# Kernel tuning notes

Measured on AMD Instinct MI355X. Metric: run time of the kernel, lower is better.

## Reference

```python
import jax, jax.numpy as jnp
import numpy as np

NEG_SLOPE = 0.2
F_OUT = 64


def setup_inputs() -> dict:
    key = jax.random.key(0)
    k1, k2, k3 = jax.random.split(key, 3)
    N, F_IN = 8192, 256
    h = jax.random.normal(k1, (N, F_IN), dtype=jnp.float32)
    adj = jnp.ones((N, N), dtype=jnp.bool_)  # unused by the original forward
    # xavier-uniform-ish init scale
    W = jax.random.uniform(k2, (F_IN, F_OUT), dtype=jnp.float32,
                           minval=-1.0, maxval=1.0) * np.sqrt(6.0 / (F_IN + F_OUT))
    a = jax.random.uniform(k3, (2 * F_OUT, 1), dtype=jnp.float32,
                           minval=-1.0, maxval=1.0) * np.sqrt(6.0 / (2 * F_OUT + 1))
    return {"h": h, "adj": adj, "W": W, "a": a}


def reference(h, adj, W, a):
    # Wh: [N, F_OUT]
    Wh = h @ W
    # The torch code materializes an [N*N, F] repeat to compute what is just
    # a broadcast add of two projected score vectors:
    # e[i, j] = leakyrelu(Wh[i] @ a1 + Wh[j] @ a2)
    s1 = Wh @ a[:F_OUT]   # [N, 1]
    s2 = Wh @ a[F_OUT:]   # [N, 1]
    e = s1 + s2.T         # [N, N]
    e = jnp.where(e >= 0, e, NEG_SLOPE * e)  # LeakyReLU(0.2)
    attention = jax.nn.softmax(e, axis=1)    # note: adj is NOT used (matches source)
    return attention @ Wh                    # [N, F_OUT]
```

## Files before the change

### kernel.cpp

```cpp
#include <hip/hip_runtime.h>
#include <math.h>

#define GN 8192
#define GF 64
#define GFIN 256
#define NEG 0.2f
#define NCH 1024
#define CHSZ 8

#define OFF_WH   0
#define OFF_S1   (GN*GF)
#define OFF_S2   (OFF_S1 + GN)
#define OFF_ZS   (OFF_S2 + GN)
#define OFF_IDX  (OFF_ZS + GN)
#define OFF_CHA  (OFF_IDX + GN)
#define OFF_CHB  (OFF_CHA + NCH*GF)
#define OFF_SCA  (OFF_CHB + NCH*GF)
#define OFF_SCB  (OFF_SCA + NCH)
#define OFF_OFA  (OFF_SCB + NCH)
#define OFF_OFB  (OFF_OFA + (NCH+1)*GF)
#define OFF_OSA  (OFF_OFB + (NCH+1)*GF)
#define OFF_OSB  (OFF_OSA + (NCH+1))

__global__ __launch_bounds__(256) void k_wh(const float* __restrict__ h,
        const float* __restrict__ W, const float* __restrict__ a,
        float* __restrict__ Wh, float* __restrict__ s1, float* __restrict__ s2) {
    __shared__ float Wl[GFIN*GF];
    int t = threadIdx.x;
    int lane = t & 63;
    const float4* W4 = (const float4*)W;
    float4* Wl4 = (float4*)Wl;
    #pragma unroll
    for (int m = 0; m < 16; ++m) Wl4[t + m*256] = W4[t + m*256];
    __syncthreads();
    int wid = __builtin_amdgcn_readfirstlane(t >> 6);
    int row0 = blockIdx.x * 32 + wid * 8;
    const float* hrow = h + (size_t)row0 * GFIN;
    float acc[8] = {0.f,0.f,0.f,0.f,0.f,0.f,0.f,0.f};
    #pragma unroll 8
    for (int k = 0; k < GFIN; ++k) {
        float wv = Wl[k*GF + lane];
        #pragma unroll
        for (int q = 0; q < 8; ++q) acc[q] += hrow[q*GFIN + k] * wv;
    }
    float a1 = a[lane], a2 = a[GF + lane];
    #pragma unroll
    for (int q = 0; q < 8; ++q) {
        int row = row0 + q;
        Wh[(size_t)row*GF + lane] = acc[q];
        float v1 = acc[q]*a1, v2 = acc[q]*a2;
        #pragma unroll
        for (int o = 32; o > 0; o >>= 1) { v1 += __shfl_xor(v1, o); v2 += __shfl_xor(v2, o); }
        if (lane == 0) { s1[row] = v1; s2[row] = v2; }
    }
}

__global__ __launch_bounds__(256) void k_rank(const float* __restrict__ s2v,
        float* __restrict__ zs, int* __restrict__ idx) {
    __shared__ float z[GN];
    int t = threadIdx.x;
    const float4* s4 = (const float4*)s2v;
    float4* z4 = (float4*)z;
    for (int m = t; m < GN/4; m += 256) z4[m] = s4[m];
    __syncthreads();
    int jl = t >> 3, s = t & 7;
    int j = blockIdx.x * 32 + jl;
    float zj = z[j];
    int cnt = 0;
    #pragma unroll 4
    for (int i = 0; i < GN/32; ++i) {
        int m4 = i*8 + s;
        float4 v = z4[m4];
        int mb = m4*4;
        cnt += (v.x < zj) || (v.x == zj && mb+0 < j);
        cnt += (v.y < zj) || (v.y == zj && mb+1 < j);
        cnt += (v.z < zj) || (v.z == zj && mb+2 < j);
        cnt += (v.w < zj) || (v.w == zj && mb+3 < j);
    }
    cnt += __shfl_xor(cnt, 1);
    cnt += __shfl_xor(cnt, 2);
    cnt += __shfl_xor(cnt, 4);
    if (s == 0) { zs[cnt] = zj; idx[cnt] = j; }
}

__global__ __launch_bounds__(256) void k_chunk(const float* __restrict__ Wh,
        const float* __restrict__ zs, const int* __restrict__ idx,
        float* __restrict__ chA, float* __restrict__ chB,
        float* __restrict__ scA, float* __restrict__ scB) {
    int t = threadIdx.x;
    int wid = t >> 6, lane = t & 63;
    int ch = blockIdx.x*4 + wid;
    float Z = zs[GN-1];
    float aAcc = 0.f, bAcc = 0.f, sa = 0.f, sb = 0.f;
    #pragma unroll
    for (int q = 0; q < CHSZ; ++q) {
        int r = ch*CHSZ + q;
        float zr = zs[r];
        int ir = idx[r];
        float d = zr - Z;
        float tA = __expf(d);
        float tB = __expf(NEG * d);
        float w = Wh[(size_t)ir*GF + lane];
        aAcc += tA*w; bAcc += tB*w; sa += tA; sb += tB;
    }
    chA[ch*GF + lane] = aAcc;
    chB[ch*GF + lane] = bAcc;
    if (lane == 0) { scA[ch] = sa; scB[ch] = sb; }
}

__global__ __launch_bounds__(256) void k_scan(const float* __restrict__ chA,
        const float* __restrict__ chB, const float* __restrict__ scA,
        const float* __restrict__ scB,
        float* __restrict__ offA, float* __restrict__ offB,
        float* __restrict__ osA, float* __restrict__ osB) {
    __shared__ float wsum[4];
    __shared__ float wsum2[4];
    int c = blockIdx.x;
    int t = threadIdx.x;
    int lane = t & 63, wid = t >> 6;
    float v[4];
    #pragma unroll
    for (int q = 0; q < 4; ++q) {
        int ch = t*4 + q;
        v[q] = (c < 64) ? chB[ch*GF + c] : scB[ch];
    }
    float s = v[0]+v[1]+v[2]+v[3];
    float ws = s;
    #pragma unroll
    for (int o = 1; o < 64; o <<= 1) { float y = __shfl_up(ws, o); if (lane >= o) ws += y; }
    if (lane == 63) wsum[wid] = ws;
    __syncthreads();
    float blkoff = 0.f, tot = 0.f;
    #pragma unroll
    for (int w2 = 0; w2 < 4; ++w2) { float x = wsum[w2]; tot += x; if (w2 < wid) blkoff += x; }
    float base = blkoff + ws - s;
    #pragma unroll
    for (int q = 0; q < 4; ++q) {
        int ch = t*4 + q;
        if (c < 64) offB[ch*GF + c] = base; else osB[ch] = base;
        base += v[q];
    }
    if (t == 0) { if (c < 64) offB[NCH*GF + c] = tot; else osB[NCH] = tot; }
    __syncthreads();
    #pragma unroll
    for (int q = 0; q < 4; ++q) {
        int ch = NCH-1 - (t*4 + q);
        v[q] = (c < 64) ? chA[ch*GF + c] : scA[ch];
    }
    s = v[0]+v[1]+v[2]+v[3];
    ws = s;
    #pragma unroll
    for (int o = 1; o < 64; o <<= 1) { float y = __shfl_up(ws, o); if (lane >= o) ws += y; }
    if (lane == 63) wsum2[wid] = ws;
    __syncthreads();
    blkoff = 0.f;
    #pragma unroll
    for (int w2 = 0; w2 < 4; ++w2) { float x = wsum2[w2]; if (w2 < wid) blkoff += x; }
    base = blkoff + ws - s;
    #pragma unroll
    for (int q = 0; q < 4; ++q) {
        int ch = NCH-1 - (t*4 + q);
        if (c < 64) offA[ch*GF + c] = base; else osA[ch] = base;
        base += v[q];
    }
    if (t == 0) { if (c < 64) offA[NCH*GF + c] = 0.f; else osA[NCH] = 0.f; }
}

__global__ __launch_bounds__(256) void k_out(const float* __restrict__ s1,
        const float* __restrict__ zs, const int* __restrict__ idx,
        const float* __restrict__ Wh,
        const float* __restrict__ offA, const float* __restrict__ offB,
        const float* __restrict__ osA, const float* __restrict__ osB,
        float* __restrict__ out) {
    int t = threadIdx.x;
    int wid = t >> 6, lane = t & 63;
    int i = blockIdx.x*4 + wid;
    float s1i = s1[i];
    float Z = zs[GN-1];
    float g = s1i + Z;
    float m = (g >= 0.f) ? g : NEG*g;
    float aA = __expf(g - m);
    float aB = __expf(NEG*g - m);
    float tgt = -s1i;
    int lo = 0, hi = GN;
    #pragma unroll
    for (int it = 0; it < 13; ++it) {
        int mid = (lo + hi) >> 1;
        if (zs[mid] < tgt) lo = mid + 1; else hi = mid;
    }
    int k = lo;
    int c0 = k >> 3;
    float va, vb, sa, pb;
    if (c0 < NCH) {
        va = offA[c0*GF + lane]; vb = offB[c0*GF + lane];
        sa = osA[c0];            pb = osB[c0];
        #pragma unroll
        for (int q = 0; q < CHSZ; ++q) {
            int r = c0*CHSZ + q;
            float zr = zs[r]; int ir = idx[r];
            float w = Wh[(size_t)ir*GF + lane];
            float d = zr - Z;
            if (r >= k) { float tA = __expf(d);      va += tA*w; sa += tA; }
            else        { float tB = __expf(NEG*d);  vb += tB*w; pb += tB; }
        }
    } else {
        va = 0.f; sa = 0.f;
        vb = offB[NCH*GF + lane]; pb = osB[NCH];
    }
    out[(size_t)i*GF + lane] = (aA*va + aB*vb) / (aA*sa + aB*pb);
}

extern "C" void kernel_launch(void* const* d_in, const int* in_sizes, int n_in,
                              void* d_out, int out_size, void* d_ws, size_t ws_size,
                              hipStream_t stream) {
    const float* h = (const float*)d_in[0];
    const float* W = (const float*)d_in[2];
    const float* a = (const float*)d_in[3];
    float* ws = (float*)d_ws;
    float* Wh  = ws + OFF_WH;
    float* s1  = ws + OFF_S1;
    float* s2  = ws + OFF_S2;
    float* zs  = ws + OFF_ZS;
    int*   idx = (int*)(ws + OFF_IDX);
    float* chA = ws + OFF_CHA;
    float* chB = ws + OFF_CHB;
    float* scA = ws + OFF_SCA;
    float* scB = ws + OFF_SCB;
    float* ofA = ws + OFF_OFA;
    float* ofB = ws + OFF_OFB;
    float* osA = ws + OFF_OSA;
    float* osB = ws + OFF_OSB;
    float* out = (float*)d_out;

    hipLaunchKernelGGL(k_wh,    dim3(GN/32),  dim3(256), 0, stream, h, W, a, Wh, s1, s2);
    hipLaunchKernelGGL(k_rank,  dim3(GN/32),  dim3(256), 0, stream, s2, zs, idx);
    hipLaunchKernelGGL(k_chunk, dim3(NCH/4),  dim3(256), 0, stream, Wh, zs, idx, chA, chB, scA, scB);
    hipLaunchKernelGGL(k_scan,  dim3(65),     dim3(256), 0, stream, chA, chB, scA, scB, ofA, ofB, osA, osB);
    hipLaunchKernelGGL(k_out,   dim3(GN/4),   dim3(256), 0, stream, s1, zs, idx, Wh, ofA, ofB, osA, osB, out);
}
```

Before: 69.81 us.

## Fuse GAT pipeline into one cooperative kernel with grid syncs

Replaces the five separate launches (projection, rank sort, chunk sums, scan, output) with one cooperative kernel of 256 blocks × 512 threads, separated by grid.sync barriers. The sorted score array is kept in LDS and reused for the chunk phase and the output binary search, which now runs with 4 rows per wavefront. Chunk size is halved (2048 chunks of 4) to shorten the per-row tail loop. This removes inter-kernel launch gaps and some global reloads, at the cost of grid-wide barrier overhead and a launch configuration limited to one block per CU.

Result: slower. 185.4 us (+165.6%).

```diff
diff --git a/kernel.cpp b/kernel.cpp
--- a/kernel.cpp
+++ b/kernel.cpp
@@ -1,12 +1,17 @@
 #include <hip/hip_runtime.h>
+#include <hip/hip_cooperative_groups.h>
 #include <math.h>
+
+namespace cg = cooperative_groups;
 
 #define GN 8192
 #define GF 64
 #define GFIN 256
 #define NEG 0.2f
-#define NCH 1024
-#define CHSZ 8
+#define NBLK 256
+#define TPB 512
+#define NCH 2048
+#define CHSZ 4
 
 #define OFF_WH   0
 #define OFF_S1   (GN*GF)
@@ -22,192 +27,203 @@
 #define OFF_OSA  (OFF_OFB + (NCH+1)*GF)
 #define OFF_OSB  (OFF_OSA + (NCH+1))
 
-__global__ __launch_bounds__(256) void k_wh(const float* __restrict__ h,
-        const float* __restrict__ W, const float* __restrict__ a,
-        float* __restrict__ Wh, float* __restrict__ s1, float* __restrict__ s2) {
-    __shared__ float Wl[GFIN*GF];
-    int t = threadIdx.x;
-    int lane = t & 63;
-    const float4* W4 = (const float4*)W;
-    float4* Wl4 = (float4*)Wl;
-    #pragma unroll
-    for (int m = 0; m < 16; ++m) Wl4[t + m*256] = W4[t + m*256];
-    __syncthreads();
-    int wid = __builtin_amdgcn_readfirstlane(t >> 6);
-    int row0 = blockIdx.x * 32 + wid * 8;
-    const float* hrow = h + (size_t)row0 * GFIN;
-    float acc[8] = {0.f,0.f,0.f,0.f,0.f,0.f,0.f,0.f};
-    #pragma unroll 8
-    for (int k = 0; k < GFIN; ++k) {
-        float wv = Wl[k*GF + lane];
-        #pragma unroll
-        for (int q = 0; q < 8; ++q) acc[q] += hrow[q*GFIN + k] * wv;
-    }
-    float a1 = a[lane], a2 = a[GF + lane];
-    #pragma unroll
-    for (int q = 0; q < 8; ++q) {
-        int row = row0 + q;
-        Wh[(size_t)row*GF + lane] = acc[q];
-        float v1 = acc[q]*a1, v2 = acc[q]*a2;
-        #pragma unroll
-        for (int o = 32; o > 0; o >>= 1) { v1 += __shfl_xor(v1, o); v2 += __shfl_xor(v2, o); }
-        if (lane == 0) { s1[row] = v1; s2[row] = v2; }
-    }
-}
-
-__global__ __launch_bounds__(256) void k_rank(const float* __restrict__ s2v,
-        float* __restrict__ zs, int* __restrict__ idx) {
-    __shared__ float z[GN];
-    int t = threadIdx.x;
-    const float4* s4 = (const float4*)s2v;
-    float4* z4 = (float4*)z;
-    for (int m = t; m < GN/4; m += 256) z4[m] = s4[m];
-    __syncthreads();
-    int jl = t >> 3, s = t & 7;
-    int j = blockIdx.x * 32 + jl;
-    float zj = z[j];
-    int cnt = 0;
-    #pragma unroll 4
-    for (int i = 0; i < GN/32; ++i) {
-        int m4 = i*8 + s;
-        float4 v = z4[m4];
-        int mb = m4*4;
-        cnt += (v.x < zj) || (v.x == zj && mb+0 < j);
-        cnt += (v.y < zj) || (v.y == zj && mb+1 < j);
-        cnt += (v.z < zj) || (v.z == zj && mb+2 < j);
-        cnt += (v.w < zj) || (v.w == zj && mb+3 < j);
-    }
-    cnt += __shfl_xor(cnt, 1);
-    cnt += __shfl_xor(cnt, 2);
-    cnt += __shfl_xor(cnt, 4);
-    if (s == 0) { zs[cnt] = zj; idx[cnt] = j; }
-}
-
-__global__ __launch_bounds__(256) void k_chunk(const float* __restrict__ Wh,
-        const float* __restrict__ zs, const int* __restrict__ idx,
-        float* __restrict__ chA, float* __restrict__ chB,
-        float* __restrict__ scA, float* __restrict__ scB) {
-    int t = threadIdx.x;
-    int wid = t >> 6, lane = t & 63;
-    int ch = blockIdx.x*4 + wid;
-    float Z = zs[GN-1];
-    float aAcc = 0.f, bAcc = 0.f, sa = 0.f, sb = 0.f;
-    #pragma unroll
-    for (int q = 0; q < CHSZ; ++q) {
-        int r = ch*CHSZ + q;
-        float zr = zs[r];
-        int ir = idx[r];
-        float d = zr - Z;
-        float tA = __expf(d);
-        float tB = __expf(NEG * d);
-        float w = Wh[(size_t)ir*GF + lane];
-        aAcc += tA*w; bAcc += tB*w; sa += tA; sb += tB;
-    }
-    chA[ch*GF + lane] = aAcc;
-    chB[ch*GF + lane] = bAcc;
-    if (lane == 0) { scA[ch] = sa; scB[ch] = sb; }
-}
-
-__global__ __launch_bounds__(256) void k_scan(const float* __restrict__ chA,
-        const float* __restrict__ chB, const float* __restrict__ scA,
-        const float* __restrict__ scB,
-        float* __restrict__ offA, float* __restrict__ offB,
-        float* __restrict__ osA, float* __restrict__ osB) {
-    __shared__ float wsum[4];
-    __shared__ float wsum2[4];
-    int c = blockIdx.x;
-    int t = threadIdx.x;
-    int lane = t & 63, wid = t >> 6;
-    float v[4];
-    #pragma unroll
-    for (int q = 0; q < 4; ++q) {
-        int ch = t*4 + q;
-        v[q] = (c < 64) ? chB[ch*GF + c] : scB[ch];
-    }
-    float s = v[0]+v[1]+v[2]+v[3];
-    float ws = s;
-    #pragma unroll
-    for (int o = 1; o < 64; o <<= 1) { float y = __shfl_up(ws, o); if (lane >= o) ws += y; }
-    if (lane == 63) wsum[wid] = ws;
-    __syncthreads();
-    float blkoff = 0.f, tot = 0.f;
-    #pragma unroll
-    for (int w2 = 0; w2 < 4; ++w2) { float x = wsum[w2]; tot += x; if (w2 < wid) blkoff += x; }
-    float base = blkoff + ws - s;
-    #pragma unroll
-    for (int q = 0; q < 4; ++q) {
-        int ch = t*4 + q;
-        if (c < 64) offB[ch*GF + c] = base; else osB[ch] = base;
-        base += v[q];
-    }
-    if (t == 0) { if (c < 64) offB[NCH*GF + c] = tot; else osB[NCH] = tot; }
-    __syncthreads();
-    #pragma unroll
-    for (int q = 0; q < 4; ++q) {
-        int ch = NCH-1 - (t*4 + q);
-        v[q] = (c < 64) ? chA[ch*GF + c] : scA[ch];
-    }
-    s = v[0]+v[1]+v[2]+v[3];
-    ws = s;
-    #pragma unroll
-    for (int o = 1; o < 64; o <<= 1) { float y = __shfl_up(ws, o); if (lane >= o) ws += y; }
-    if (lane == 63) wsum2[wid] = ws;
-    __syncthreads();
-    blkoff = 0.f;
-    #pragma unroll
-    for (int w2 = 0; w2 < 4; ++w2) { float x = wsum2[w2]; if (w2 < wid) blkoff += x; }
-    base = blkoff + ws - s;
-    #pragma unroll
-    for (int q = 0; q < 4; ++q) {
-        int ch = NCH-1 - (t*4 + q);
-        if (c < 64) offA[ch*GF + c] = base; else osA[ch] = base;
-        base += v[q];
-    }
-    if (t == 0) { if (c < 64) offA[NCH*GF + c] = 0.f; else osA[NCH] = 0.f; }
-}
-
-__global__ __launch_bounds__(256) void k_out(const float* __restrict__ s1,
-        const float* __restrict__ zs, const int* __restrict__ idx,
-        const float* __restrict__ Wh,
-        const float* __restrict__ offA, const float* __restrict__ offB,
-        const float* __restrict__ osA, const float* __restrict__ osB,
+__global__ __launch_bounds__(TPB) void k_gat(
+        const float* __restrict__ h, const float* __restrict__ W,
+        const float* __restrict__ a, float* __restrict__ wsf,
         float* __restrict__ out) {
-    int t = threadIdx.x;
-    int wid = t >> 6, lane = t & 63;
-    int i = blockIdx.x*4 + wid;
-    float s1i = s1[i];
-    float Z = zs[GN-1];
-    float g = s1i + Z;
-    float m = (g >= 0.f) ? g : NEG*g;
-    float aA = __expf(g - m);
-    float aB = __expf(NEG*g - m);
-    float tgt = -s1i;
-    int lo = 0, hi = GN;
-    #pragma unroll
-    for (int it = 0; it < 13; ++it) {
-        int mid = (lo + hi) >> 1;
-        if (zs[mid] < tgt) lo = mid + 1; else hi = mid;
-    }
-    int k = lo;
-    int c0 = k >> 3;
-    float va, vb, sa, pb;
-    if (c0 < NCH) {
-        va = offA[c0*GF + lane]; vb = offB[c0*GF + lane];
-        sa = osA[c0];            pb = osB[c0];
+    cg::grid_group grid = cg::this_grid();
+    __shared__ float lds[GFIN*GF];
+
+    float* Wh  = wsf + OFF_WH;
+    float* s1  = wsf + OFF_S1;
+    float* s2  = wsf + OFF_S2;
+    float* zs  = wsf + OFF_ZS;
+    int*   idx = (int*)(wsf + OFF_IDX);
+    float* chA = wsf + OFF_CHA;
+    float* chB = wsf + OFF_CHB;
+    float* scA = wsf + OFF_SCA;
+    float* scB = wsf + OFF_SCB;
+    float* ofA = wsf + OFF_OFA;
+    float* ofB = wsf + OFF_OFB;
+    float* osA = wsf + OFF_OSA;
+    float* osB = wsf + OFF_OSB;
+
+    int t = threadIdx.x, lane = t & 63;
+    int b = blockIdx.x;
+
+    {
+        const float4* W4 = (const float4*)W;
+        float4* l4 = (float4*)lds;
+        #pragma unroll
+        for (int m = 0; m < 8; ++m) l4[t + m*TPB] = W4[t + m*TPB];
+        __syncthreads();
+        int wid = __builtin_amdgcn_readfirstlane(t >> 6);
+        int row0 = b*32 + wid*4;
+        const float* hrow = h + (size_t)row0 * GFIN;
+        float acc[4] = {0.f,0.f,0.f,0.f};
+        #pragma unroll 8
+        for (int k = 0; k < GFIN; ++k) {
+            float wv = lds[k*GF + lane];
+            #pragma unroll
+            for (int q = 0; q < 4; ++q) acc[q] += hrow[q*GFIN + k] * wv;
+        }
+        float a1 = a[lane], a2 = a[GF + lane];
+        #pragma unroll
+        for (int q = 0; q < 4; ++q) {
+            int row = row0 + q;
+            Wh[(size_t)row*GF + lane] = acc[q];
+            float v1 = acc[q]*a1, v2 = acc[q]*a2;
+            #pragma unroll
+            for (int o = 32; o > 0; o >>= 1) { v1 += __shfl_xor(v1, o); v2 += __shfl_xor(v2, o); }
+            if (lane == 0) { s1[row] = v1; s2[row] = v2; }
+        }
+    }
+    grid.sync();
+    {
+        float4* z4 = (float4*)lds;
+        const float4* s4 = (const float4*)s2;
+        for (int m = t; m < GN/4; m += TPB) z4[m] = s4[m];
+        __syncthreads();
+        int jl = t >> 4, sl = t & 15;
+        int j = b*32 + jl;
+        float zj = lds[j];
+        int cnt = 0;
+        #pragma unroll 4
+        for (int i = 0; i < GN/64; ++i) {
+            int m4 = i*16 + sl;
+            float4 v = z4[m4];
+            int mb = m4*4;
+            cnt += (v.x < zj) || (v.x == zj && mb   < j);
+            cnt += (v.y < zj) || (v.y == zj && mb+1 < j);
+            cnt += (v.z < zj) || (v.z == zj && mb+2 < j);
+            cnt += (v.w < zj) || (v.w == zj && mb+3 < j);
+        }
+        cnt += __shfl_xor(cnt, 1);
+        cnt += __shfl_xor(cnt, 2);
+        cnt += __shfl_xor(cnt, 4);
+        cnt += __shfl_xor(cnt, 8);
+        if (sl == 0) { zs[cnt] = zj; idx[cnt] = j; }
+    }
+    grid.sync();
+    {
+        float4* z4 = (float4*)lds;
+        const float4* g4 = (const float4*)zs;
+        for (int m = t; m < GN/4; m += TPB) z4[m] = g4[m];
+        __syncthreads();
+        float Z = lds[GN-1];
+        int wid = __builtin_amdgcn_readfirstlane(t >> 6);
+        int ch = b*8 + wid;
+        const int* ip = idx + ch*CHSZ;
+        float aAcc = 0.f, bAcc = 0.f, sa = 0.f, sb = 0.f;
         #pragma unroll
         for (int q = 0; q < CHSZ; ++q) {
-            int r = c0*CHSZ + q;
-            float zr = zs[r]; int ir = idx[r];
+            int r = ch*CHSZ + q;
+            float zr = lds[r];
+            int ir = ip[q];
+            float d = zr - Z;
+            float tA = __expf(d);
+            float tB = __expf(NEG * d);
             float w = Wh[(size_t)ir*GF + lane];
-            float d = zr - Z;
-            if (r >= k) { float tA = __expf(d);      va += tA*w; sa += tA; }
-            else        { float tB = __expf(NEG*d);  vb += tB*w; pb += tB; }
-        }
-    } else {
-        va = 0.f; sa = 0.f;
-        vb = offB[NCH*GF + lane]; pb = osB[NCH];
-    }
-    out[(size_t)i*GF + lane] = (aA*va + aB*vb) / (aA*sa + aB*pb);
+            aAcc += tA*w; bAcc += tB*w; sa += tA; sb += tB;
+        }
+        chA[ch*GF + lane] = aAcc;
+        chB[ch*GF + lane] = bAcc;
+        if (lane == 0) { scA[ch] = sa; scB[ch] = sb; }
+    }
+    grid.sync();
+    if (b < 65) {
+        float* wred  = lds + 8192;
+        float* wredA = lds + 8208;
+        int wid = t >> 6;
+        int c = b;
+        float v[4];
+        #pragma unroll
+        for (int q = 0; q < 4; ++q) { int ch = t*4 + q; v[q] = (c < 64) ? chB[ch*GF + c] : scB[ch]; }
+        float s = v[0]+v[1]+v[2]+v[3];
+        float wsc = s;
+        #pragma unroll
+        for (int o = 1; o < 64; o <<= 1) { float y = __shfl_up(wsc, o); if (lane >= o) wsc += y; }
+        if (lane == 63) wred[wid] = wsc;
+        __syncthreads();
+        float blkoff = 0.f, tot = 0.f;
+        #pragma unroll
+        for (int w2 = 0; w2 < 8; ++w2) { float x = wred[w2]; tot += x; if (w2 < wid) blkoff += x; }
+        float base = blkoff + wsc - s;
+        #pragma unroll
+        for (int q = 0; q < 4; ++q) {
+            int ch = t*4 + q;
+            if (c < 64) ofB[ch*GF + c] = base; else osB[ch] = base;
+            base += v[q];
+        }
+        if (t == 0) { if (c < 64) ofB[NCH*GF + c] = tot; else osB[NCH] = tot; }
+        #pragma unroll
+        for (int q = 0; q < 4; ++q) { int ch = NCH-1 - (t*4 + q); v[q] = (c < 64) ? chA[ch*GF + c] : scA[ch]; }
+        s = v[0]+v[1]+v[2]+v[3];
+        wsc = s;
+        #pragma unroll
+        for (int o = 1; o < 64; o <<= 1) { float y = __shfl_up(wsc, o); if (lane >= o) wsc += y; }
+        if (lane == 63) wredA[wid] = wsc;
+        __syncthreads();
+        blkoff = 0.f;
+        #pragma unroll
+        for (int w2 = 0; w2 < 8; ++w2) { float x = wredA[w2]; if (w2 < wid) blkoff += x; }
+        base = blkoff + wsc - s;
+        #pragma unroll
+        for (int q = 0; q < 4; ++q) {
+            int ch = NCH-1 - (t*4 + q);
+            if (c < 64) ofA[ch*GF + c] = base; else osA[ch] = base;
+            base += v[q];
+        }
+        if (t == 0) { if (c < 64) ofA[NCH*GF + c] = 0.f; else osA[NCH] = 0.f; }
+    }
+    grid.sync();
+    {
+        float Z = lds[GN-1];
+        int wid = t >> 6;
+        int r0 = b*32 + wid*4;
+        float s1v[4], g[4], mm[4], aA[4], aB[4];
+        int lo[4], hi[4];
+        #pragma unroll
+        for (int q = 0; q < 4; ++q) {
+            s1v[q] = s1[r0 + q]; lo[q] = 0; hi[q] = GN;
+            g[q] = s1v[q] + Z;
+            mm[q] = (g[q] >= 0.f) ? g[q] : NEG*g[q];
+            aA[q] = __expf(g[q] - mm[q]);
+            aB[q] = __expf(NEG*g[q] - mm[q]);
+        }
+        #pragma unroll
+        for (int it = 0; it < 13; ++it) {
+            #pragma unroll
+            for (int q = 0; q < 4; ++q) {
+                int mid = (lo[q] + hi[q]) >> 1;
+                if (lds[mid] < -s1v[q]) lo[q] = mid + 1; else hi[q] = mid;
+            }
+        }
+        #pragma unroll
+        for (int q = 0; q < 4; ++q) {
+            int k = lo[q];
+            int c0 = __builtin_amdgcn_readfirstlane(k >> 2);
+            float va, vb, sa, pb;
+            if (c0 < NCH) {
+                va = ofA[c0*GF + lane]; vb = ofB[c0*GF + lane];
+                sa = osA[c0];           pb = osB[c0];
+                const int* ip = idx + c0*CHSZ;
+                #pragma unroll
+                for (int qq = 0; qq < CHSZ; ++qq) {
+                    int r = c0*CHSZ + qq;
+                    float zr = lds[r]; int ir = ip[qq];
+                    float w = Wh[(size_t)ir*GF + lane];
+                    float d = zr - Z;
+                    if (r >= k) { float tA = __expf(d);     va += tA*w; sa += tA; }
+                    else        { float tB = __expf(NEG*d); vb += tB*w; pb += tB; }
+                }
+            } else {
+                va = 0.f; sa = 0.f;
+                vb = ofB[NCH*GF + lane]; pb = osB[NCH];
+            }
+            out[(size_t)(r0+q)*GF + lane] = (aA[q]*va + aB[q]*vb) / (aA[q]*sa + aB[q]*pb);
+        }
+    }
 }
 
 extern "C" void kernel_launch(void* const* d_in, const int* in_sizes, int n_in,
@@ -216,25 +232,9 @@
     const float* h = (const float*)d_in[0];
     const float* W = (const float*)d_in[2];
     const float* a = (const float*)d_in[3];
-    float* ws = (float*)d_ws;
-    float* Wh  = ws + OFF_WH;
-    float* s1  = ws + OFF_S1;
-    float* s2  = ws + OFF_S2;
-    float* zs  = ws + OFF_ZS;
-    int*   idx = (int*)(ws + OFF_IDX);
-    float* chA = ws + OFF_CHA;
-    float* chB = ws + OFF_CHB;
-    float* scA = ws + OFF_SCA;
-    float* scB = ws + OFF_SCB;
-    float* ofA = ws + OFF_OFA;
-    float* ofB = ws + OFF_OFB;
-    float* osA = ws + OFF_OSA;
-    float* osB = ws + OFF_OSB;
+    float* wsf = (float*)d_ws;
     float* out = (float*)d_out;
-
-    hipLaunchKernelGGL(k_wh,    dim3(GN/32),  dim3(256), 0, stream, h, W, a, Wh, s1, s2);
-    hipLaunchKernelGGL(k_rank,  dim3(GN/32),  dim3(256), 0, stream, s2, zs, idx);
-    hipLaunchKernelGGL(k_chunk, dim3(NCH/4),  dim3(256), 0, stream, Wh, zs, idx, chA, chB, scA, scB);
-    hipLaunchKernelGGL(k_scan,  dim3(65),     dim3(256), 0, stream, chA, chB, scA, scB, ofA, ofB, osA, osB);
-    hipLaunchKernelGGL(k_out,   dim3(GN/4),   dim3(256), 0, stream, s1, zs, idx, Wh, ofA, ofB, osA, osB, out);
+    void* args[] = { (void*)&h, (void*)&W, (void*)&a, (void*)&wsf, (void*)&out };
+    hipLaunchCooperativeKernel(reinterpret_cast<void*>(k_gat),
+                               dim3(NBLK), dim3(TPB), args, 0, stream);
 }
```
